# Optimization experiments

Measured on AMD Instinct MI355X. Metric: run time of the kernel, lower is better.

Reference implementation:

```python
import jax, jax.numpy as jnp
import numpy as np

B, S, SE, D, H, F1, I, E, ND = 8, 512, 512, 1024, 16, 4096, 1024, 8, 4

def _ln(x, g, b, eps=1e-5):
    mu = x.mean(-1, keepdims=True)
    var = ((x - mu) ** 2).mean(-1, keepdims=True)
    return (x - mu) * jax.lax.rsqrt(var + eps) * g + b

def _mha(q_in, kv_in, qw, qb, kw, kb, vw, vb, ow, ob):
    b, sq, d = q_in.shape
    sk = kv_in.shape[1]
    dh = d // H
    scale = dh ** -0.5
    q = ((q_in @ qw.T + qb) * scale).reshape(b, sq, H, dh)
    k = (kv_in @ kw.T + kb).reshape(b, sk, H, dh)
    v = (kv_in @ vw.T + vb).reshape(b, sk, H, dh)
    attn = jax.nn.softmax(jnp.einsum('bqhd,bkhd->bhqk', q, k), axis=-1)
    o = jnp.einsum('bhqk,bkhd->bqhd', attn, v).reshape(b, sq, d)
    return o @ ow.T + ob

def setup_inputs():
    key = jax.random.key(0)
    ks = jax.random.split(key, 40)
    p = lambda i, sh: jax.random.normal(ks[i], sh, jnp.float32) * 0.02
    return {
        'hidden_states': jax.random.normal(ks[0], (B, S, D), jnp.float32),
        'encoder_hidden_states': jax.random.normal(ks[1], (B, SE, D), jnp.float32),
        'idxes': jax.random.randint(ks[2], (B,), 0, ND),
        'sa_qw': p(3, (D, D)), 'sa_qb': p(4, (D,)), 'sa_kw': p(5, (D, D)), 'sa_kb': p(6, (D,)),
        'sa_vw': p(7, (D, D)), 'sa_vb': p(8, (D,)), 'sa_ow': p(9, (D, D)), 'sa_ob': p(10, (D,)),
        'ca_qw': p(11, (D, D)), 'ca_qb': p(12, (D,)), 'ca_kw': p(13, (D, D)), 'ca_kb': p(14, (D,)),
        'ca_vw': p(15, (D, D)), 'ca_vb': p(16, (D,)), 'ca_ow': p(17, (D, D)), 'ca_ob': p(18, (D,)),
        'sa_ln_g': jnp.ones((D,), jnp.float32), 'sa_ln_b': jnp.zeros((D,), jnp.float32),
        'ca_ln_g': jnp.ones((D,), jnp.float32), 'ca_ln_b': jnp.zeros((D,), jnp.float32),
        'fin_ln_g': jnp.ones((D,), jnp.float32), 'fin_ln_b': jnp.zeros((D,), jnp.float32),
        'fc1_w': p(19, (F1, D)), 'fc1_b': p(20, (F1,)),
        'fc2_w': p(21, (D, F1)), 'fc2_b': p(22, (D,)),
        'exp1_w': p(23, (E, I, D)), 'exp1_b': p(24, (E, I)),
        'exp2_w': p(25, (E, D, I)),
        'gate_w': p(26, (ND, E, D)), 'gate_b': p(27, (ND, E)),
    }

def reference(hidden_states, encoder_hidden_states, idxes, sa_qw, sa_qb, sa_kw, sa_kb, sa_vw, sa_vb, sa_ow, sa_ob, ca_qw, ca_qb, ca_kw, ca_kb, ca_vw, ca_vb, ca_ow, ca_ob, sa_ln_g, sa_ln_b, ca_ln_g, ca_ln_b, fin_ln_g, fin_ln_b, fc1_w, fc1_b, fc2_w, fc2_b, exp1_w, exp1_b, exp2_w, gate_w, gate_b):
    # self-attention block
    res = hidden_states
    h = _mha(hidden_states, hidden_states, sa_qw, sa_qb, sa_kw, sa_kb, sa_vw, sa_vb, sa_ow, sa_ob)
    h = _ln(res + h, sa_ln_g, sa_ln_b)
    # cross-attention block
    res = h
    h = _mha(h, encoder_hidden_states, ca_qw, ca_qb, ca_kw, ca_kb, ca_vw, ca_vb, ca_ow, ca_ob)
    h = _ln(res + h, ca_ln_g, ca_ln_b)
    # dataset-gated MoE FFN (dropout=0 eval, margin_loss=False, keep_resident=True)
    bsz, seq, d = h.shape
    x = h.reshape(-1, d)                              # [T, D]
    tok_ds = jnp.repeat(idxes, seq)                   # [T] dataset id per token
    logits = jnp.einsum('ted,td->te', gate_w[tok_ds], x) + gate_b[tok_ds]
    probs = jax.nn.softmax(logits, axis=-1)
    gate = jnp.argmax(probs, axis=-1)                 # top-1 expert per token
    gate_value = jnp.max(probs, axis=-1)
    oh = jax.nn.one_hot(gate, E, dtype=x.dtype)       # [T, E] dispatch mask
    # effective expert fc1 = concat(fc1, expert_fc1): shared half + per-token expert half
    h1 = jax.nn.gelu(x @ fc1_w.T + fc1_b, approximate=False)                                  # [T, F1]
    h2 = jax.nn.gelu(jnp.einsum('td,te,eid->ti', x, oh, exp1_w) + exp1_b[gate], approximate=False)  # [T, I]
    # effective expert fc2 = concat(fc2, expert_fc2, dim=1), shared fc2 bias
    out = h1 @ fc2_w.T + jnp.einsum('ti,te,edi->td', h2, oh, exp2_w) + fc2_b                  # [T, D]
    out = out * gate_value[:, None]                   # keep_resident: scale before residual
    out = _ln(x + out, fin_ln_g, fin_ln_b)
    return out.reshape(bsz, seq, d)
```

## Files before the change

kernel.cpp:

```cpp
#include <hip/hip_runtime.h>
#include <math.h>

constexpr int cS = 512, cD = 1024, cH = 16, cDH = 64;
constexpr int cF1 = 4096, cI = 1024, cE = 8;
constexpr int cT = 4096;
constexpr long long TD = (long long)cT * cD;
constexpr long long WW = 1048576;

typedef __attribute__((ext_vector_type(8))) short bfrag;
typedef _Float16 f16x8 __attribute__((ext_vector_type(8)));
typedef __attribute__((ext_vector_type(4))) float f32x4;

__device__ __forceinline__ float gelu_exact(float x) {
  return 0.5f * x * (1.0f + erff(x * 0.70710678118654752440f));
}
__device__ __forceinline__ unsigned short f2b_rne(float x) {
  union { float f; unsigned u; } v; v.f = x;
  unsigned r = v.u + 0x7fffu + ((v.u >> 16) & 1u);
  return (unsigned short)(r >> 16);
}
__device__ __forceinline__ void split2(float v, unsigned short& h, unsigned short& m) {
  _Float16 hh = (_Float16)v;
  float r = v - (float)hh;
  _Float16 mm = (_Float16)r;
  union { _Float16 f; unsigned short u; } a, b;
  a.f = hh; b.f = mm;
  h = a.u; m = b.u;
}
__device__ __forceinline__ void async16(const void* g, void* l) {
  __builtin_amdgcn_global_load_lds(
      (const __attribute__((address_space(1))) unsigned int*)g,
      (__attribute__((address_space(3))) unsigned int*)l, 16, 0, 0);
}
__device__ __forceinline__ float wsum(float v) {
#pragma unroll
  for (int off = 32; off; off >>= 1) v += __shfl_xor(v, off, 64);
  return v;
}
__device__ __forceinline__ float wmax(float v) {
#pragma unroll
  for (int off = 32; off; off >>= 1) v = fmaxf(v, __shfl_xor(v, off, 64));
  return v;
}
__device__ __forceinline__ int swzoff(int R, int c) {
  const int r = R & 15;
  return (R >> 4) * 512 + (r >> 1) * 64 + (((((r & 1) << 2) | c) ^ ((r >> 1) & 7)) << 3);
}

template<int BM, int BN, int NW, int WR, int OUT_MODE>
__global__ __launch_bounds__(NW * 64) void mgemm2(
    const unsigned short* __restrict__ Ap, long long aPS, long long sA, int lda,
    const unsigned short* __restrict__ Bp, long long bPS, long long sB, int ldb,
    const float* __restrict__ bias,
    void* __restrict__ Cp, long long sC, int ldc,
    int K, float alpha, int zbase)
{
  constexpr int WC = NW / WR;
  constexpr int WM = BM / WR, WN = BN / WC, AI = WM / 16, BJ = WN / 16;
  constexpr int CA = 2 * (BM / 16);
  constexpr int CB = 2 * (BN / 16);
  constexpr int CTOT = CA + CB;
  static_assert(CTOT % NW == 0, "chunk count");
  constexpr int NCH = CTOT / NW;
  constexpr int LT = (BM + BN) * 64;

  __shared__ unsigned short lds[2][LT];

  const int tid = threadIdx.x;
  const int w = tid >> 6, lane = tid & 63;
  const int z = blockIdx.z;
  const int m0 = blockIdx.x * BM, n0 = blockIdx.y * BN;
  const int wm = (w / WC) * WM, wn = (w % WC) * WN;
  const int sp = (lane & 7) ^ ((lane >> 3) & 7);
  const int srow = ((lane >> 3) << 1) | (sp >> 2);
  const int scol = (sp & 3) << 3;

  const unsigned short* gsrc[NCH];
  int loff[NCH];
#pragma unroll
  for (int ci = 0; ci < NCH; ++ci) {
    const int c = w + ci * NW;
    if (c < CA) {
      const int p = c / (BM / 16), cc = c % (BM / 16);
      const int row = cc * 16 + srow;
      gsrc[ci] = Ap + p * aPS + (long long)z * sA + (long long)(m0 + row) * lda + scol;
      loff[ci] = p * (BM * 32) + cc * 512;
    } else {
      const int cb = c - CA;
      const int p = cb / (BN / 16), cc = cb % (BN / 16);
      const int row = cc * 16 + srow;
      gsrc[ci] = Bp + p * bPS + (long long)z * sB + (long long)(n0 + row) * ldb + scol;
      loff[ci] = 2 * (BM * 32) + p * (BN * 32) + cc * 512;
    }
  }

  f32x4 acc[AI][BJ];
#pragma unroll
  for (int i = 0; i < AI; ++i)
#pragma unroll
    for (int j = 0; j < BJ; ++j) acc[i][j] = (f32x4){0.f, 0.f, 0.f, 0.f};

#pragma unroll
  for (int ci = 0; ci < NCH; ++ci) async16(gsrc[ci], &lds[0][loff[ci]]);
  asm volatile("s_waitcnt vmcnt(0)" ::: "memory");
  __syncthreads();

  int cur = 0;
  const int lc = lane >> 4;
  for (int k0 = 32; k0 <= K; k0 += 32) {
    if (k0 < K) {
#pragma unroll
      for (int ci = 0; ci < NCH; ++ci) async16(gsrc[ci] + k0, &lds[cur ^ 1][loff[ci]]);
    }
    const unsigned short* LA0 = &lds[cur][0];
    const unsigned short* LA1 = &lds[cur][BM * 32];
    const unsigned short* LB0 = &lds[cur][2 * (BM * 32)];
    const unsigned short* LB1 = &lds[cur][2 * (BM * 32) + BN * 32];

    f16x8 bf0[BJ], bf1[BJ], af[AI];
#pragma unroll
    for (int j = 0; j < BJ; ++j) {
      bf0[j] = *(const f16x8*)&LB0[swzoff(wn + j * 16 + (lane & 15), lc)];
      bf1[j] = *(const f16x8*)&LB1[swzoff(wn + j * 16 + (lane & 15), lc)];
    }
#pragma unroll
    for (int i = 0; i < AI; ++i)
      af[i] = *(const f16x8*)&LA0[swzoff(wm + i * 16 + (lane & 15), lc)];
    __builtin_amdgcn_s_setprio(1);
#pragma unroll
    for (int i = 0; i < AI; ++i)
#pragma unroll
      for (int j = 0; j < BJ; ++j)
        acc[i][j] = __builtin_amdgcn_mfma_f32_16x16x32_f16(af[i], bf0[j], acc[i][j], 0, 0, 0);
#pragma unroll
    for (int i = 0; i < AI; ++i)
#pragma unroll
      for (int j = 0; j < BJ; ++j)
        acc[i][j] = __builtin_amdgcn_mfma_f32_16x16x32_f16(af[i], bf1[j], acc[i][j], 0, 0, 0);
    __builtin_amdgcn_s_setprio(0);
#pragma unroll
    for (int i = 0; i < AI; ++i)
      af[i] = *(const f16x8*)&LA1[swzoff(wm + i * 16 + (lane & 15), lc)];
    __builtin_amdgcn_s_setprio(1);
#pragma unroll
    for (int i = 0; i < AI; ++i)
#pragma unroll
      for (int j = 0; j < BJ; ++j)
        acc[i][j] = __builtin_amdgcn_mfma_f32_16x16x32_f16(af[i], bf0[j], acc[i][j], 0, 0, 0);
    __builtin_amdgcn_s_setprio(0);
    asm volatile("s_waitcnt vmcnt(0)" ::: "memory");
    __syncthreads();
    cur ^= 1;
  }

#pragma unroll
  for (int i = 0; i < AI; ++i) {
#pragma unroll
    for (int r = 0; r < 4; ++r) {
      const int gm = m0 + wm + i * 16 + (lane >> 4) * 4 + r;
#pragma unroll
      for (int j = 0; j < BJ; ++j) {
        const int gn = n0 + wn + j * 16 + (lane & 15);
        float v = acc[i][j][r];
        if constexpr (OUT_MODE == 4) {
          const int tsel = gn >> 10, gnn = gn & 1023;
          v += bias[tsel * cD + gnn];
          unsigned short* C = (unsigned short*)Cp + (long long)(zbase + tsel) * 2 * TD;
          const int b = gm >> 9, s = gm & 511, h = gnn >> 6, dd = gnn & 63;
          const long long idx = (((long long)(b * cH + h) * cS + s) << 6) + dd;
          unsigned short h_, m_;
          split2(v, h_, m_);
          C[idx] = h_; C[TD + idx] = m_;
        } else if constexpr (OUT_MODE == 5) {
          const int zz = zbase + z;
          const int b = zz >> 4, h = zz & 15;
          const long long idx = ((long long)(b * cS + gm) << 10) + h * 64 + gn;
          unsigned short h_, m_;
          split2(v, h_, m_);
          ((unsigned short*)Cp)[idx] = h_;
          ((unsigned short*)Cp)[sC + idx] = m_;
        } else {
          if (bias) v += bias[gn];
          v *= alpha;
          const long long idx = (long long)z * sC + (long long)gm * ldc + gn;
          ((float*)Cp)[idx] = v;
        }
      }
    }
  }
}

__global__ __launch_bounds__(256) void transposeV(
    const unsigned short* __restrict__ src, unsigned short* __restrict__ dst)
{
  __shared__ unsigned short t[128 * 64];
  const int st = blockIdx.x;
  const int bh = blockIdx.y;
  const long long pl = (long long)blockIdx.z * TD;
  const unsigned short* Sp = src + pl + ((long long)bh * cS + st * 128) * cDH;
  const int tid = threadIdx.x;
  const int r0 = tid >> 3, c0 = (tid & 7) * 8;
#pragma unroll
  for (int i = 0; i < 4; ++i) {
    const int r = r0 + i * 32;
    uint4 v = *(const uint4*)(Sp + (long long)r * cDH + c0);
    *(uint4*)&t[r * 64 + (c0 ^ ((r & 7) << 3))] = v;
  }
  __syncthreads();
  const int dd = tid >> 2;
  unsigned short* Dp = dst + pl + (long long)(bh * cDH + dd) * cS + st * 128;
#pragma unroll
  for (int i = 0; i < 4; ++i) {
    const int s0 = ((tid & 3) + i * 4) * 8;
    alignas(16) unsigned short v[8];
#pragma unroll
    for (int j = 0; j < 8; ++j)
      v[j] = t[(s0 + j) * 64 + (dd ^ (j << 3))];
    *(uint4*)(Dp + s0) = *(const uint4*)v;
  }
}

template<int GATHER>
__global__ __launch_bounds__(256) void mgemm1(
    const unsigned short* __restrict__ A, int lda,
    const unsigned short* __restrict__ Bw, long long sB, int ldb,
    const float* __restrict__ bias, int sBias,
    void* __restrict__ Cp, int ldc,
    int K, int act, int obf, int accum,
    const int* __restrict__ token_list, const int* __restrict__ offsets)
{
  int m0, n0, beg = 0, cnt = 0x7fffffff;
  long long boff = 0;
  if constexpr (GATHER) {
    const int e = blockIdx.y;
    beg = offsets[e]; cnt = offsets[e + 1] - beg;
    m0 = blockIdx.z * 128;
    if (m0 >= cnt) return;
    n0 = blockIdx.x * 128;
    boff = (long long)e * sB;
    if (bias) bias += (long long)e * sBias;
  } else {
    m0 = blockIdx.x * 128; n0 = blockIdx.y * 128;
  }
  __shared__ unsigned short lds[2][256 * 32];
  const int tid = threadIdx.x, w = tid >> 6, lane = tid & 63;
  const int wm = (w >> 1) * 64, wn = (w & 1) * 64;
  const int sp = (lane & 7) ^ ((lane >> 3) & 7);
  const int srow = ((lane >> 3) << 1) | (sp >> 2);
  const int scol = (sp & 3) << 3;

  const unsigned short* gsrc[4];
  int loff[4];
#pragma unroll
  for (int ci = 0; ci < 4; ++ci) {
    const int c = w + ci * 4;
    if (c < 8) {
      const int row = c * 16 + srow;
      long long grow;
      if constexpr (GATHER) {
        int mr = m0 + row; if (mr >= cnt) mr = cnt - 1;
        grow = token_list[beg + mr];
      } else grow = m0 + row;
      gsrc[ci] = A + grow * (long long)lda + scol;
      loff[ci] = c * 512;
    } else {
      const int cc = c - 8;
      const int row = cc * 16 + srow;
      gsrc[ci] = Bw + boff + (long long)(n0 + row) * ldb + scol;
      loff[ci] = 128 * 32 + cc * 512;
    }
  }
  f32x4 acc[4][4];
#pragma unroll
  for (int i = 0; i < 4; ++i)
#pragma unroll
    for (int j = 0; j < 4; ++j) acc[i][j] = (f32x4){0.f, 0.f, 0.f, 0.f};

#pragma unroll
  for (int ci = 0; ci < 4; ++ci) async16(gsrc[ci], &lds[0][loff[ci]]);
  asm volatile("s_waitcnt vmcnt(0)" ::: "memory");
  __syncthreads();

  int cur = 0;
  const int lc = lane >> 4;
  for (int k0 = 32; k0 <= K; k0 += 32) {
    if (k0 < K) {
#pragma unroll
      for (int ci = 0; ci < 4; ++ci) async16(gsrc[ci] + k0, &lds[cur ^ 1][loff[ci]]);
    }
    const unsigned short* lA = &lds[cur][0];
    const unsigned short* lB = &lds[cur][128 * 32];
    bfrag af[4], bf[4];
#pragma unroll
    for (int i = 0; i < 4; ++i)
      af[i] = *(const bfrag*)&lA[swzoff(wm + i * 16 + (lane & 15), lc)];
#pragma unroll
    for (int j = 0; j < 4; ++j)
      bf[j] = *(const bfrag*)&lB[swzoff(wn + j * 16 + (lane & 15), lc)];
    __builtin_amdgcn_s_setprio(1);
#pragma unroll
    for (int i = 0; i < 4; ++i)
#pragma unroll
      for (int j = 0; j < 4; ++j)
        acc[i][j] = __builtin_amdgcn_mfma_f32_16x16x32_bf16(af[i], bf[j], acc[i][j], 0, 0, 0);
    __builtin_amdgcn_s_setprio(0);
    asm volatile("s_waitcnt vmcnt(0)" ::: "memory");
    __syncthreads();
    cur ^= 1;
  }

#pragma unroll
  for (int i = 0; i < 4; ++i) {
#pragma unroll
    for (int r = 0; r < 4; ++r) {
      const int ml = wm + i * 16 + (lane >> 4) * 4 + r;
      long long orow = 0; bool ok = true;
      if constexpr (GATHER) {
        if (m0 + ml < cnt) orow = token_list[beg + m0 + ml]; else ok = false;
      } else orow = m0 + ml;
      if (ok) {
#pragma unroll
        for (int j = 0; j < 4; ++j) {
          const int gn = n0 + wn + j * 16 + (lane & 15);
          float v = acc[i][j][r];
          if (bias) v += bias[gn];
          if (act) v = gelu_exact(v);
          const long long idx = orow * (long long)ldc + gn;
          if (obf) ((unsigned short*)Cp)[idx] = f2b_rne(v);
          else if (accum) ((float*)Cp)[idx] += v;
          else ((float*)Cp)[idx] = v;
        }
      }
    }
  }
}

__global__ __launch_bounds__(256) void softmax2(
    const float* __restrict__ Sc, unsigned short* __restrict__ P, long long pPS)
{
  const int w = threadIdx.x >> 6, lane = threadIdx.x & 63;
  const long long row = (long long)blockIdx.x * 4 + w;
  const float* pr = Sc + row * cS + lane * 8;
  float4 a = *(const float4*)pr;
  float4 b = *(const float4*)(pr + 4);
  float e[8] = {a.x, a.y, a.z, a.w, b.x, b.y, b.z, b.w};
  float m = e[0];
#pragma unroll
  for (int q = 1; q < 8; ++q) m = fmaxf(m, e[q]);
  m = wmax(m);
  float s = 0.f;
#pragma unroll
  for (int q = 0; q < 8; ++q) { e[q] = expf(e[q] - m); s += e[q]; }
  s = wsum(s);
  const float inv = 1.0f / s;
  unsigned h[4], mm[4];
#pragma unroll
  for (int q = 0; q < 4; ++q) {
    unsigned short h0, m0s, h1, m1s;
    split2(e[2 * q] * inv, h0, m0s);
    split2(e[2 * q + 1] * inv, h1, m1s);
    h[q] = (unsigned)h0 | ((unsigned)h1 << 16);
    mm[q] = (unsigned)m0s | ((unsigned)m1s << 16);
  }
  const long long o = row * cS + lane * 8;
  *(uint4*)&P[o] = *(const uint4*)h;
  *(uint4*)&P[pPS + o] = *(const uint4*)mm;
}

__global__ __launch_bounds__(256) void addln_kernel(
    const float* __restrict__ ra, const float* __restrict__ rb,
    const float* __restrict__ rowscale,
    const float* __restrict__ g, const float* __restrict__ be,
    float* __restrict__ out, unsigned short* __restrict__ out16,
    unsigned short* __restrict__ out2p,
    int gate_on, const int* __restrict__ idxes,
    const float* __restrict__ gw, const float* __restrict__ gb,
    int* __restrict__ gate_idx, float* __restrict__ gate_val, int* __restrict__ counts)
{
  const int w = threadIdx.x >> 6, lane = threadIdx.x & 63;
  const int row = blockIdx.x * 4 + w;
  const long long base = (long long)row * cD + lane * 16;
  const float sc = rowscale ? rowscale[row] : 1.0f;
  float v[16];
#pragma unroll
  for (int q = 0; q < 4; ++q) {
    float4 a = *(const float4*)(ra + base + q * 4);
    float4 b = *(const float4*)(rb + base + q * 4);
    v[q * 4 + 0] = a.x + b.x * sc; v[q * 4 + 1] = a.y + b.y * sc;
    v[q * 4 + 2] = a.z + b.z * sc; v[q * 4 + 3] = a.w + b.w * sc;
  }
  float s = 0.f;
#pragma unroll
  for (int q = 0; q < 16; ++q) s += v[q];
  const float mu = wsum(s) * (1.0f / cD);
  float vp = 0.f;
#pragma unroll
  for (int q = 0; q < 16; ++q) { float c = v[q] - mu; vp += c * c; }
  const float rstd = 1.0f / sqrtf(wsum(vp) * (1.0f / cD) + 1e-5f);
  float x[16];
#pragma unroll
  for (int q = 0; q < 4; ++q) {
    float4 gv = *(const float4*)(g + lane * 16 + q * 4);
    float4 bv = *(const float4*)(be + lane * 16 + q * 4);
    x[q * 4 + 0] = (v[q * 4 + 0] - mu) * rstd * gv.x + bv.x;
    x[q * 4 + 1] = (v[q * 4 + 1] - mu) * rstd * gv.y + bv.y;
    x[q * 4 + 2] = (v[q * 4 + 2] - mu) * rstd * gv.z + bv.z;
    x[q * 4 + 3] = (v[q * 4 + 3] - mu) * rstd * gv.w + bv.w;
  }
  if (out) {
#pragma unroll
    for (int q = 0; q < 4; ++q) {
      float4 o; o.x = x[q * 4]; o.y = x[q * 4 + 1]; o.z = x[q * 4 + 2]; o.w = x[q * 4 + 3];
      *(float4*)(out + base + q * 4) = o;
    }
  }
  if (out16) {
    unsigned u[8];
#pragma unroll
    for (int q = 0; q < 8; ++q)
      u[q] = (unsigned)f2b_rne(x[2 * q]) | ((unsigned)f2b_rne(x[2 * q + 1]) << 16);
    *(uint4*)&out16[base] = *(const uint4*)&u[0];
    *(uint4*)&out16[base + 8] = *(const uint4*)&u[4];
  }
  if (out2p) {
    unsigned uh[8], um[8];
#pragma unroll
    for (int q = 0; q < 8; ++q) {
      unsigned short h0, m0s, h1, m1s;
      split2(x[2 * q], h0, m0s);
      split2(x[2 * q + 1], h1, m1s);
      uh[q] = (unsigned)h0 | ((unsigned)h1 << 16);
      um[q] = (unsigned)m0s | ((unsigned)m1s << 16);
    }
    *(uint4*)&out2p[base] = *(const uint4*)&uh[0];
    *(uint4*)&out2p[base + 8] = *(const uint4*)&uh[4];
    *(uint4*)&out2p[TD + base] = *(const uint4*)&um[0];
    *(uint4*)&out2p[TD + base + 8] = *(const uint4*)&um[4];
  }
  if (gate_on) {
    const int ds = idxes[row >> 9];
    const float* gwr = gw + (long long)ds * (cE * cD) + lane * 16;
    float glog[8];
#pragma unroll
    for (int e = 0; e < 8; ++e) {
      float pe = 0.f;
#pragma unroll
      for (int q = 0; q < 4; ++q) {
        float4 wv = *(const float4*)(gwr + e * cD + q * 4);
        pe += x[q * 4] * wv.x + x[q * 4 + 1] * wv.y + x[q * 4 + 2] * wv.z + x[q * 4 + 3] * wv.w;
      }
      glog[e] = wsum(pe);
    }
    if (lane == 0) {
      float m = glog[0] + gb[ds * cE];
      int arg = 0;
      float gl[8];
      gl[0] = m;
#pragma unroll
      for (int e = 1; e < 8; ++e) {
        gl[e] = glog[e] + gb[ds * cE + e];
        if (gl[e] > m) { m = gl[e]; arg = e; }
      }
      float ssum = 0.f;
#pragma unroll
      for (int e = 0; e < 8; ++e) ssum += expf(gl[e] - m);
      gate_idx[row] = arg;
      gate_val[row] = 1.0f / ssum;
      atomicAdd(&counts[arg], 1);
    }
  }
}

__global__ __launch_bounds__(256) void conv2x4(
    const float* s0, const float* s1, const float* s2, const float* s3,
    unsigned short* dst, int n, float sc0)
{
  const int wsel = blockIdx.y;
  const float* s = (wsel == 0) ? s0 : (wsel == 1) ? s1 : (wsel == 2) ? s2 : s3;
  const float sc = (wsel == 0) ? sc0 : 1.0f;
  unsigned short* dh = dst + (long long)(wsel < 3 ? wsel : 6) * n;
  unsigned short* dm = dh + (long long)(wsel < 3 ? 3 : 1) * n;
  const long long i = ((long long)blockIdx.x * 256 + threadIdx.x) * 4;
  if (i >= n) return;
  float4 v = *(const float4*)(s + i);
  float vv[4] = {v.x * sc, v.y * sc, v.z * sc, v.w * sc};
  unsigned short h[4], m[4];
#pragma unroll
  for (int q = 0; q < 4; ++q) split2(vv[q], h[q], m[q]);
  uint2 u;
  u.x = (unsigned)h[0] | ((unsigned)h[1] << 16); u.y = (unsigned)h[2] | ((unsigned)h[3] << 16);
  *(uint2*)&dh[i] = u;
  u.x = (unsigned)m[0] | ((unsigned)m[1] << 16); u.y = (unsigned)m[2] | ((unsigned)m[3] << 16);
  *(uint2*)&dm[i] = u;
}

__global__ __launch_bounds__(256) void conv2p(const float* __restrict__ s,
                                              unsigned short* __restrict__ d, long long n)
{
  const long long i = ((long long)blockIdx.x * 256 + threadIdx.x) * 4;
  if (i >= n) return;
  float4 v = *(const float4*)(s + i);
  unsigned short h[4], m[4];
  split2(v.x, h[0], m[0]); split2(v.y, h[1], m[1]);
  split2(v.z, h[2], m[2]); split2(v.w, h[3], m[3]);
  uint2 u;
  u.x = (unsigned)h[0] | ((unsigned)h[1] << 16); u.y = (unsigned)h[2] | ((unsigned)h[3] << 16);
  *(uint2*)&d[i] = u;
  u.x = (unsigned)m[0] | ((unsigned)m[1] << 16); u.y = (unsigned)m[2] | ((unsigned)m[3] << 16);
  *(uint2*)&d[n + i] = u;
}

__global__ __launch_bounds__(256) void conv1(const float* __restrict__ s,
                                             unsigned short* __restrict__ d, long long n)
{
  const long long i = ((long long)blockIdx.x * 256 + threadIdx.x) * 4;
  if (i >= n) return;
  float4 v = *(const float4*)(s + i);
  uint2 u;
  u.x = (unsigned)f2b_rne(v.x) | ((unsigned)f2b_rne(v.y) << 16);
  u.y = (unsigned)f2b_rne(v.z) | ((unsigned)f2b_rne(v.w) << 16);
  *(uint2*)&d[i] = u;
}

__global__ void prep_bias(const float* a0, const float* a1, const float* a2,
                          const float* b0, const float* b1, const float* b2,
                          float* dst)
{
  const int i = blockIdx.x * 256 + threadIdx.x;
  const int seg = i >> 10, off = i & 1023;
  const float* srcs[6] = {a0, a1, a2, b0, b1, b2};
  const float sc = (seg == 0 || seg == 3) ? 0.125f : 1.0f;
  dst[i] = srcs[seg][off] * sc;
}

__global__ void scan_kernel(const int* __restrict__ counts, int* __restrict__ offsets,
                            int* __restrict__ cursor)
{
  if (threadIdx.x == 0 && blockIdx.x == 0) {
    int a = 0;
    for (int e = 0; e < cE; ++e) { offsets[e] = a; cursor[e] = a; a += counts[e]; }
    offsets[cE] = a;
  }
}

__global__ __launch_bounds__(256) void scatter_kernel(
    const int* __restrict__ gate_idx, int* __restrict__ cursor, int* __restrict__ token_list)
{
  int t = blockIdx.x * 256 + threadIdx.x;
  if (t < cT) {
    int e = gate_idx[t];
    int slot = atomicAdd(&cursor[e], 1);
    token_list[slot] = t;
  }
}

extern "C" void kernel_launch(void* const* d_in, const int* in_sizes, int n_in,
                              void* d_out, int out_size, void* d_ws, size_t ws_size,
                              hipStream_t stream)
{
  (void)in_sizes; (void)n_in; (void)out_size;
  const float* hidden  = (const float*)d_in[0];
  const float* encoder = (const float*)d_in[1];
  const int*   idxes   = (const int*)d_in[2];
  const float* sa_qw = (const float*)d_in[3];
  const float* sa_qb = (const float*)d_in[4];
  const float* sa_kw = (const float*)d_in[5];
  const float* sa_kb = (const float*)d_in[6];
  const float* sa_vw = (const float*)d_in[7];
  const float* sa_vb = (const float*)d_in[8];
  const float* sa_ow = (const float*)d_in[9];
  const float* sa_ob = (const float*)d_in[10];
  const float* ca_qw = (const float*)d_in[11];
  const float* ca_qb = (const float*)d_in[12];
  const float* ca_kw = (const float*)d_in[13];
  const float* ca_kb = (const float*)d_in[14];
  const float* ca_vw = (const float*)d_in[15];
  const float* ca_vb = (const float*)d_in[16];
  const float* ca_ow = (const float*)d_in[17];
  const float* ca_ob = (const float*)d_in[18];
  const float* sa_ln_g = (const float*)d_in[19];
  const float* sa_ln_b = (const float*)d_in[20];
  const float* ca_ln_g = (const float*)d_in[21];
  const float* ca_ln_b = (const float*)d_in[22];
  const float* fin_ln_g = (const float*)d_in[23];
  const float* fin_ln_b = (const float*)d_in[24];
  const float* fc1_w = (const float*)d_in[25];
  const float* fc1_b = (const float*)d_in[26];
  const float* fc2_w = (const float*)d_in[27];
  const float* fc2_b = (const float*)d_in[28];
  const float* exp1_w = (const float*)d_in[29];
  const float* exp1_b = (const float*)d_in[30];
  const float* exp2_w = (const float*)d_in[31];
  const float* gate_w = (const float*)d_in[32];
  const float* gate_b = (const float*)d_in[33];
  float* out = (float*)d_out;

  size_t off = 0;
  auto alloc = [&](size_t bytes) {
    void* p = (char*)d_ws + off;
    off += (bytes + 255) & ~(size_t)255;
    return p;
  };
  unsigned short* wbuf = (unsigned short*)alloc(4ll * 2 * WW * 2);
  unsigned short* QKVs = (unsigned short*)alloc(4ll * 2 * TD * 2);
  unsigned short* attnO16 = (unsigned short*)alloc(2ll * TD * 2);
  float* hsa   = (float*)alloc(TD * 4);
  float* biasb = (float*)alloc(6 * cD * 4);
  float* gate_val = (float*)alloc(cT * 4);
  int* gate_idx   = (int*)alloc(cT * 4);
  int* token_list = (int*)alloc(cT * 4);
  int* ctl        = (int*)alloc(64 * 4);
  int* counts  = ctl;
  int* offsets = ctl + 16;
  int* cursor  = ctl + 32;
  const size_t off_x = off;
  float* xbuf = (float*)alloc(TD * 4);
  unsigned short* x16 = (unsigned short*)alloc(TD * 2);

  long long region_bytes = (long long)ws_size - (long long)off_x;
  long long perz = (long long)cS * cS * 8;
  int ZB = (int)(region_bytes / perz);
  if (ZB < 1) ZB = 1;
  if (ZB > 128) ZB = 128;
  float* scoresF = (float*)((char*)d_ws + off_x);
  unsigned short* Pp = (unsigned short*)((char*)d_ws + off_x + (long long)ZB * cS * cS * 4);
  const long long pPS = (long long)ZB * cS * cS;

  unsigned short* A16 = QKVs + 6 * TD;
  unsigned short* hsa16 = attnO16;
  float* OdeltaF = (float*)QKVs;
  unsigned short* h2 = QKVs;
  float* moeF = (float*)(QKVs + 2 * WW * 4);
  unsigned short* h1 = QKVs + 16ll * WW;

  dim3 blk(256), blk512(512);
  hipMemsetAsync(counts, 0, cE * sizeof(int), stream);
  prep_bias<<<dim3(24), blk, 0, stream>>>(sa_qb, sa_kb, sa_vb, ca_qb, ca_kb, ca_vb, biasb);

  auto attention = [&]() {
    for (int zb = 0; zb < 128; zb += ZB) {
      int zc = 128 - zb; if (zc > ZB) zc = ZB;
      mgemm2<64, 256, 4, 1, 0><<<dim3(8, 2, zc), blk, 0, stream>>>(
          QKVs + (long long)zb * (cS * cDH), TD, (long long)cS * cDH, cDH,
          QKVs + 2 * TD + (long long)zb * (cS * cDH), TD, (long long)cS * cDH, cDH,
          nullptr, scoresF, (long long)cS * cS, cS, cDH, 1.0f, 0);
      softmax2<<<dim3(zc * cS / 4), blk, 0, stream>>>(scoresF, Pp, pPS);
      mgemm2<128, 64, 4, 2, 5><<<dim3(4, 1, zc), blk, 0, stream>>>(
          Pp, pPS, (long long)cS * cS, cS,
          QKVs + 6 * TD + (long long)zb * (cDH * cS), TD, (long long)cDH * cS, cS,
          nullptr, attnO16, TD, 0, cS, 1.0f, zb);
    }
  };

  conv2x4<<<dim3(1024, 4), blk, 0, stream>>>(sa_qw, sa_kw, sa_vw, sa_ow, wbuf, (int)WW, 0.125f);
  conv2p<<<dim3(4096), blk, 0, stream>>>(hidden, A16, TD);
  mgemm2<128, 192, 8, 2, 4><<<dim3(32, 16, 1), blk512, 0, stream>>>(
      A16, TD, 0, cD, wbuf, 3 * WW, 0, cD,
      biasb, QKVs, 0, 0, cD, 1.0f, 0);
  transposeV<<<dim3(4, 128, 2), blk, 0, stream>>>(QKVs + 4 * TD, QKVs + 6 * TD);
  attention();
  mgemm2<128, 128, 4, 2, 0><<<dim3(32, 8, 1), blk, 0, stream>>>(
      attnO16, TD, 0, cD, wbuf + 6ll * WW, WW, 0, cD,
      sa_ob, OdeltaF, 0, cD, cD, 1.0f, 0);
  addln_kernel<<<dim3(cT / 4), blk, 0, stream>>>(
      hidden, OdeltaF, nullptr, sa_ln_g, sa_ln_b, hsa, nullptr, hsa16,
      0, nullptr, nullptr, nullptr, nullptr, nullptr, nullptr);

  conv2x4<<<dim3(1024, 4), blk, 0, stream>>>(ca_qw, ca_kw, ca_vw, ca_ow, wbuf, (int)WW, 0.125f);
  mgemm2<128, 128, 4, 2, 4><<<dim3(32, 8, 1), blk, 0, stream>>>(
      hsa16, TD, 0, cD, wbuf, 3 * WW, 0, cD,
      biasb + 3 * cD, QKVs, 0, 0, cD, 1.0f, 0);
  conv2p<<<dim3(4096), blk, 0, stream>>>(encoder, A16, TD);
  mgemm2<128, 128, 4, 2, 4><<<dim3(32, 16, 1), blk, 0, stream>>>(
      A16, TD, 0, cD, wbuf + WW, 3 * WW, 0, cD,
      biasb + 4 * cD, QKVs, 0, 0, cD, 1.0f, 1);
  transposeV<<<dim3(4, 128, 2), blk, 0, stream>>>(QKVs + 4 * TD, QKVs + 6 * TD);
  attention();
  mgemm2<128, 128, 4, 2, 0><<<dim3(32, 8, 1), blk, 0, stream>>>(
      attnO16, TD, 0, cD, wbuf + 6ll * WW, WW, 0, cD,
      ca_ob, OdeltaF, 0, cD, cD, 1.0f, 0);
  addln_kernel<<<dim3(cT / 4), blk, 0, stream>>>(
      hsa, OdeltaF, nullptr, ca_ln_g, ca_ln_b, xbuf, x16, nullptr,
      1, idxes, gate_w, gate_b, gate_idx, gate_val, counts);

  scan_kernel<<<dim3(1), dim3(64), 0, stream>>>(counts, offsets, cursor);
  scatter_kernel<<<dim3(16), blk, 0, stream>>>(gate_idx, cursor, token_list);

  unsigned short* wfc1 = wbuf;
  unsigned short* wfc2 = wbuf + 4194304;
  conv1<<<dim3(4096), blk, 0, stream>>>(fc1_w, wfc1, 4194304);
  conv1<<<dim3(4096), blk, 0, stream>>>(fc2_w, wfc2, 4194304);
  mgemm1<0><<<dim3(32, 32), blk, 0, stream>>>(
      x16, cD, wfc1, 0, cD, fc1_b, 0,
      h1, cF1, cD, 1, 1, 0, nullptr, nullptr);
  mgemm1<0><<<dim3(32, 8), blk, 0, stream>>>(
      h1, cF1, wfc2, 0, cF1, fc2_b, 0,
      moeF, cD, cF1, 0, 0, 0, nullptr, nullptr);
  conv1<<<dim3(8192), blk, 0, stream>>>(exp1_w, wbuf, 8388608);
  mgemm1<1><<<dim3(8, 8, 32), blk, 0, stream>>>(
      x16, cD, wbuf, (long long)cI * cD, cD, exp1_b, cI,
      h2, cI, cD, 1, 1, 0, token_list, offsets);
  conv1<<<dim3(8192), blk, 0, stream>>>(exp2_w, wbuf, 8388608);
  mgemm1<1><<<dim3(8, 8, 32), blk, 0, stream>>>(
      h2, cI, wbuf, (long long)cD * cI, cI, nullptr, 0,
      moeF, cD, cI, 0, 0, 1, token_list, offsets);

  addln_kernel<<<dim3(cT / 4), blk, 0, stream>>>(
      xbuf, moeF, gate_val, fin_ln_g, fin_ln_b, out, nullptr, nullptr,
      0, nullptr, nullptr, nullptr, nullptr, nullptr, nullptr);
}
```

Before: 1.126 ms.

## Triple-buffer GEMM LDS pipeline with partial vmcnt waits and retile launches

Both GEMM kernels move from double-buffered LDS with a full vmcnt(0) wait plus barrier each iteration to a three-stage ring. Two tiles are prefetched up front, and each iteration waits only for the oldest tile's loads before a single barrier. Several mgemm2 launches also change to 64x128 tiles, which doubles the block count for better CU occupancy. The costs are 1.5x LDS per block, which can lower occupancy, and more fragile wait counts tied to NCH.

```diff
diff --git a/kernel.cpp b/kernel.cpp
--- a/kernel.cpp
+++ b/kernel.cpp
@@ -31,6 +31,15 @@
   __builtin_amdgcn_global_load_lds(
       (const __attribute__((address_space(1))) unsigned int*)g,
       (__attribute__((address_space(3))) unsigned int*)l, 16, 0, 0);
+}
+template<int N> __device__ __forceinline__ void vwait() {
+  if constexpr (N == 0)       asm volatile("s_waitcnt vmcnt(0)" ::: "memory");
+  else if constexpr (N == 4)  asm volatile("s_waitcnt vmcnt(4)" ::: "memory");
+  else if constexpr (N == 5)  asm volatile("s_waitcnt vmcnt(5)" ::: "memory");
+  else if constexpr (N == 6)  asm volatile("s_waitcnt vmcnt(6)" ::: "memory");
+  else if constexpr (N == 8)  asm volatile("s_waitcnt vmcnt(8)" ::: "memory");
+  else if constexpr (N == 10) asm volatile("s_waitcnt vmcnt(10)" ::: "memory");
+  else static_assert(N == 0, "unsupported vmcnt");
 }
 __device__ __forceinline__ float wsum(float v) {
 #pragma unroll
@@ -64,7 +73,7 @@
   constexpr int NCH = CTOT / NW;
   constexpr int LT = (BM + BN) * 64;
 
-  __shared__ unsigned short lds[2][LT];
+  __shared__ unsigned short lds[3][LT];
 
   const int tid = threadIdx.x;
   const int w = tid >> 6, lane = tid & 63;
@@ -100,22 +109,26 @@
 #pragma unroll
     for (int j = 0; j < BJ; ++j) acc[i][j] = (f32x4){0.f, 0.f, 0.f, 0.f};
 
+  const int NK = K >> 5;
 #pragma unroll
   for (int ci = 0; ci < NCH; ++ci) async16(gsrc[ci], &lds[0][loff[ci]]);
-  asm volatile("s_waitcnt vmcnt(0)" ::: "memory");
-  __syncthreads();
-
-  int cur = 0;
+#pragma unroll
+  for (int ci = 0; ci < NCH; ++ci) async16(gsrc[ci] + 32, &lds[1][loff[ci]]);
+
+  int cr = 0, cw = 2;
   const int lc = lane >> 4;
-  for (int k0 = 32; k0 <= K; k0 += 32) {
-    if (k0 < K) {
-#pragma unroll
-      for (int ci = 0; ci < NCH; ++ci) async16(gsrc[ci] + k0, &lds[cur ^ 1][loff[ci]]);
-    }
-    const unsigned short* LA0 = &lds[cur][0];
-    const unsigned short* LA1 = &lds[cur][BM * 32];
-    const unsigned short* LB0 = &lds[cur][2 * (BM * 32)];
-    const unsigned short* LB1 = &lds[cur][2 * (BM * 32) + BN * 32];
+  for (int t = 0; t < NK; ++t) {
+    if (t + 1 < NK) vwait<NCH>(); else vwait<0>();
+    __builtin_amdgcn_s_barrier();
+    if (t + 2 < NK) {
+      const int k0 = (t + 2) * 32;
+#pragma unroll
+      for (int ci = 0; ci < NCH; ++ci) async16(gsrc[ci] + k0, &lds[cw][loff[ci]]);
+    }
+    const unsigned short* LA0 = &lds[cr][0];
+    const unsigned short* LA1 = &lds[cr][BM * 32];
+    const unsigned short* LB0 = &lds[cr][2 * (BM * 32)];
+    const unsigned short* LB1 = &lds[cr][2 * (BM * 32) + BN * 32];
 
     f16x8 bf0[BJ], bf1[BJ], af[AI];
 #pragma unroll
@@ -148,9 +161,8 @@
       for (int j = 0; j < BJ; ++j)
         acc[i][j] = __builtin_amdgcn_mfma_f32_16x16x32_f16(af[i], bf0[j], acc[i][j], 0, 0, 0);
     __builtin_amdgcn_s_setprio(0);
-    asm volatile("s_waitcnt vmcnt(0)" ::: "memory");
-    __syncthreads();
-    cur ^= 1;
+    cr = (cr == 2) ? 0 : cr + 1;
+    cw = (cw == 2) ? 0 : cw + 1;
   }
 
 #pragma unroll
@@ -242,7 +254,7 @@
   } else {
     m0 = blockIdx.x * 128; n0 = blockIdx.y * 128;
   }
-  __shared__ unsigned short lds[2][256 * 32];
+  __shared__ unsigned short lds[3][256 * 32];
   const int tid = threadIdx.x, w = tid >> 6, lane = tid & 63;
   const int wm = (w >> 1) * 64, wn = (w & 1) * 64;
   const int sp = (lane & 7) ^ ((lane >> 3) & 7);
@@ -276,20 +288,24 @@
 #pragma unroll
     for (int j = 0; j < 4; ++j) acc[i][j] = (f32x4){0.f, 0.f, 0.f, 0.f};
 
+  const int NK = K >> 5;
 #pragma unroll
   for (int ci = 0; ci < 4; ++ci) async16(gsrc[ci], &lds[0][loff[ci]]);
-  asm volatile("s_waitcnt vmcnt(0)" ::: "memory");
-  __syncthreads();
-
-  int cur = 0;
+#pragma unroll
+  for (int ci = 0; ci < 4; ++ci) async16(gsrc[ci] + 32, &lds[1][loff[ci]]);
+
+  int cr = 0, cw = 2;
   const int lc = lane >> 4;
-  for (int k0 = 32; k0 <= K; k0 += 32) {
-    if (k0 < K) {
-#pragma unroll
-      for (int ci = 0; ci < 4; ++ci) async16(gsrc[ci] + k0, &lds[cur ^ 1][loff[ci]]);
-    }
-    const unsigned short* lA = &lds[cur][0];
-    const unsigned short* lB = &lds[cur][128 * 32];
+  for (int t = 0; t < NK; ++t) {
+    if (t + 1 < NK) vwait<4>(); else vwait<0>();
+    __builtin_amdgcn_s_barrier();
+    if (t + 2 < NK) {
+      const int k0 = (t + 2) * 32;
+#pragma unroll
+      for (int ci = 0; ci < 4; ++ci) async16(gsrc[ci] + k0, &lds[cw][loff[ci]]);
+    }
+    const unsigned short* lA = &lds[cr][0];
+    const unsigned short* lB = &lds[cr][128 * 32];
     bfrag af[4], bf[4];
 #pragma unroll
     for (int i = 0; i < 4; ++i)
@@ -304,9 +320,8 @@
       for (int j = 0; j < 4; ++j)
         acc[i][j] = __builtin_amdgcn_mfma_f32_16x16x32_bf16(af[i], bf[j], acc[i][j], 0, 0, 0);
     __builtin_amdgcn_s_setprio(0);
-    asm volatile("s_waitcnt vmcnt(0)" ::: "memory");
-    __syncthreads();
-    cur ^= 1;
+    cr = (cr == 2) ? 0 : cr + 1;
+    cw = (cw == 2) ? 0 : cw + 1;
   }
 
 #pragma unroll
@@ -640,7 +655,7 @@
   auto attention = [&]() {
     for (int zb = 0; zb < 128; zb += ZB) {
       int zc = 128 - zb; if (zc > ZB) zc = ZB;
-      mgemm2<64, 256, 4, 1, 0><<<dim3(8, 2, zc), blk, 0, stream>>>(
+      mgemm2<64, 128, 4, 1, 0><<<dim3(8, 4, zc), blk, 0, stream>>>(
           QKVs + (long long)zb * (cS * cDH), TD, (long long)cS * cDH, cDH,
           QKVs + 2 * TD + (long long)zb * (cS * cDH), TD, (long long)cS * cDH, cDH,
           nullptr, scoresF, (long long)cS * cS, cS, cDH, 1.0f, 0);
@@ -659,7 +674,7 @@
       biasb, QKVs, 0, 0, cD, 1.0f, 0);
   transposeV<<<dim3(4, 128, 2), blk, 0, stream>>>(QKVs + 4 * TD, QKVs + 6 * TD);
   attention();
-  mgemm2<128, 128, 4, 2, 0><<<dim3(32, 8, 1), blk, 0, stream>>>(
+  mgemm2<64, 128, 4, 1, 0><<<dim3(64, 8, 1), blk, 0, stream>>>(
       attnO16, TD, 0, cD, wbuf + 6ll * WW, WW, 0, cD,
       sa_ob, OdeltaF, 0, cD, cD, 1.0f, 0);
   addln_kernel<<<dim3(cT / 4), blk, 0, stream>>>(
@@ -667,16 +682,16 @@
       0, nullptr, nullptr, nullptr, nullptr, nullptr, nullptr);
 
   conv2x4<<<dim3(1024, 4), blk, 0, stream>>>(ca_qw, ca_kw, ca_vw, ca_ow, wbuf, (int)WW, 0.125f);
-  mgemm2<128, 128, 4, 2, 4><<<dim3(32, 8, 1), blk, 0, stream>>>(
+  mgemm2<64, 128, 4, 1, 4><<<dim3(64, 8, 1), blk, 0, stream>>>(
       hsa16, TD, 0, cD, wbuf, 3 * WW, 0, cD,
       biasb + 3 * cD, QKVs, 0, 0, cD, 1.0f, 0);
   conv2p<<<dim3(4096), blk, 0, stream>>>(encoder, A16, TD);
-  mgemm2<128, 128, 4, 2, 4><<<dim3(32, 16, 1), blk, 0, stream>>>(
+  mgemm2<64, 128, 4, 1, 4><<<dim3(64, 16, 1), blk, 0, stream>>>(
       A16, TD, 0, cD, wbuf + WW, 3 * WW, 0, cD,
       biasb + 4 * cD, QKVs, 0, 0, cD, 1.0f, 1);
   transposeV<<<dim3(4, 128, 2), blk, 0, stream>>>(QKVs + 4 * TD, QKVs + 6 * TD);
   attention();
-  mgemm2<128, 128, 4, 2, 0><<<dim3(32, 8, 1), blk, 0, stream>>>(
+  mgemm2<64, 128, 4, 1, 0><<<dim3(64, 8, 1), blk, 0, stream>>>(
       attnO16, TD, 0, cD, wbuf + 6ll * WW, WW, 0, cD,
       ca_ob, OdeltaF, 0, cD, cD, 1.0f, 0);
   addln_kernel<<<dim3(cT / 4), blk, 0, stream>>>(
```

After: 1.229 ms. 9.2% more time.
